# Kernel tuning notes

Measured on AMD Instinct MI355X. Metric: run time of the kernel, lower is better.

The kernel has to match this reference:

```python
import jax, jax.numpy as jnp
import numpy as np

N = 50000        # nodes
E = 800000       # edges (avg degree 16)
D_IN = 128
D_OUT = 128
P_DROP = 0.1
BN_EPS = 1e-5


def setup_inputs() -> dict:
    key = jax.random.key(0)
    k1, k2, k3 = jax.random.split(key, 3)
    x = jax.random.normal(k1, (N, D_IN), dtype=jnp.float32)
    edge_index = jax.random.randint(k2, (2, E), 0, N, dtype=jnp.int64)
    W = jax.random.normal(k3, (D_IN, D_OUT), dtype=jnp.float32) / np.sqrt(D_IN).astype(np.float32)
    b = jnp.zeros((D_OUT,), jnp.float32)
    bn_gamma = jnp.ones((D_OUT,), jnp.float32)
    bn_beta = jnp.zeros((D_OUT,), jnp.float32)
    return {"x": x, "edge_index": edge_index, "W": W, "b": b,
            "bn_gamma": bn_gamma, "bn_beta": bn_beta}


def reference(x, edge_index, W, b, bn_gamma, bn_beta):
    n = x.shape[0]
    # --- GCNConv: h = x W, symmetric-normalized aggregation with self-loops ---
    h = x @ W                                            # [N, D_OUT]
    loops = jnp.arange(n, dtype=edge_index.dtype)
    src = jnp.concatenate([edge_index[0], loops])        # [E+N]
    dst = jnp.concatenate([edge_index[1], loops])        # [E+N]
    deg = jax.ops.segment_sum(jnp.ones_like(dst, h.dtype), dst, num_segments=n)
    dinv = jax.lax.rsqrt(jnp.maximum(deg, 1.0))          # deg >= 1 (self-loops)
    norm = dinv[src] * dinv[dst]                         # [E+N]
    msg = h[src] * norm[:, None]                         # gather + weight
    z = jax.ops.segment_sum(msg, dst, num_segments=n) + b
    # --- activation ---
    z = jax.nn.relu(z)
    # --- BatchNorm over nodes (training-mode batch statistics) ---
    mean = z.mean(axis=0)
    var = z.var(axis=0)
    z = bn_gamma * (z - mean) * jax.lax.rsqrt(var + BN_EPS) + bn_beta
    # --- dropout (training mode, fixed key for determinism) ---
    keep = jax.random.bernoulli(jax.random.key(42), 1.0 - P_DROP, z.shape)
    z = jnp.where(keep, z / (1.0 - P_DROP), 0.0)
    return z.astype(x.dtype)
```

## Files before the change

kernel.cpp:

```cpp
#include <hip/hip_runtime.h>
#include <stdint.h>


#define NN 50000
#define NE 800000
#define DD 128
#define SCAN_B 256
#define NSB ((NN + SCAN_B - 1) / SCAN_B)
#define NSTAT 400

using f32x4  = __attribute__((ext_vector_type(4))) float;
using short8 = __attribute__((ext_vector_type(8))) short;

__device__ __forceinline__ uint32_t rotl32(uint32_t x, uint32_t d) {
  return (x << d) | (x >> (32u - d));
}

__device__ __forceinline__ uint32_t threefry_bits(uint32_t idx) {
  const uint32_t ks0 = 0u;
  const uint32_t ks1 = 42u;
  const uint32_t ks2 = 0x1BD11BDAu ^ ks0 ^ ks1;
  uint32_t x0 = ks0;
  uint32_t x1 = idx + ks1;
#define TF_R(r) { x0 += x1; x1 = rotl32(x1, (r)); x1 ^= x0; }
  TF_R(13u) TF_R(15u) TF_R(26u) TF_R(6u)
  x0 += ks1; x1 += ks2 + 1u;
  TF_R(17u) TF_R(29u) TF_R(16u) TF_R(24u)
  x0 += ks2; x1 += ks0 + 2u;
  TF_R(13u) TF_R(15u) TF_R(26u) TF_R(6u)
  x0 += ks0; x1 += ks1 + 3u;
  TF_R(17u) TF_R(29u) TF_R(16u) TF_R(24u)
  x0 += ks1; x1 += ks2 + 4u;
  TF_R(13u) TF_R(15u) TF_R(26u) TF_R(6u)
  x0 += ks2; x1 += ks0 + 5u;
#undef TF_R
  return x0 ^ x1;
}

__device__ __forceinline__ uint32_t f2bf(float f) {
  uint32_t u = __float_as_uint(f);
  return (u + 0x7fffu + ((u >> 16) & 1u)) >> 16;
}
__device__ __forceinline__ float bf2f(uint32_t h) { return __uint_as_float(h << 16); }
__device__ __forceinline__ float bf_lo(uint32_t p) { return __uint_as_float(p << 16); }
__device__ __forceinline__ float bf_hi(uint32_t p) { return __uint_as_float(p & 0xffff0000u); }

__global__ __launch_bounds__(256) void k_wpack(const float* __restrict__ Wm,
                                               short8* __restrict__ wfh,
                                               short8* __restrict__ wfl) {
  int tid = blockIdx.x * 256 + threadIdx.x;
  if (tid >= 32 * 64) return;
  int lane = tid & 63;
  int cfks = tid >> 6;
  int ks = cfks >> 3, cf = cfks & 7;
  int krow = ks * 32 + ((lane >> 4) << 3);
  int col = cf * 16 + (lane & 15);
  short8 h, l;
#pragma unroll
  for (int j = 0; j < 8; ++j) {
    float w = Wm[(size_t)(krow + j) * DD + col];
    uint32_t hb = f2bf(w);
    uint32_t lb = f2bf(w - bf2f(hb));
    h[j] = (short)hb;
    l[j] = (short)lb;
  }
  wfh[tid] = h;
  wfl[tid] = l;
}

#define GBM 128
__global__ __launch_bounds__(256) void k_gemm(const float* __restrict__ x,
                                              const short8* __restrict__ wfh,
                                              const short8* __restrict__ wfl,
                                              const float* __restrict__ dinv,
                                              uint16_t* __restrict__ hbf) {
  __shared__ uint4 ldsbuf[4096];
  char* lds = (char*)ldsbuf;
  const int t = threadIdx.x;
  const int row0 = blockIdx.x * GBM;
  const int c4 = t & 31, rbase = t >> 5;

#pragma unroll
  for (int i = 0; i < 16; ++i) {
    int r = rbase + i * 8;
    int grow = row0 + r;
    float4 v = make_float4(0.f, 0.f, 0.f, 0.f);
    if (grow < NN)
      v = *reinterpret_cast<const float4*>(&x[(size_t)grow * DD + c4 * 4]);
    uint32_t h0 = f2bf(v.x), h1 = f2bf(v.y), h2 = f2bf(v.z), h3 = f2bf(v.w);
    uint32_t l0 = f2bf(v.x - bf2f(h0)), l1 = f2bf(v.y - bf2f(h1));
    uint32_t l2 = f2bf(v.z - bf2f(h2)), l3 = f2bf(v.w - bf2f(h3));
    int byte = (r * 256 + c4 * 8) ^ ((r & 7) << 4);
    *reinterpret_cast<uint2*>(lds + byte) = make_uint2(h0 | (h1 << 16), h2 | (h3 << 16));
    *reinterpret_cast<uint2*>(lds + 32768 + byte) = make_uint2(l0 | (l1 << 16), l2 | (l3 << 16));
  }
  __syncthreads();

  const int wv = t >> 6, l = t & 63;
  f32x4 acc[2][8] = {};
#pragma unroll
  for (int ks = 0; ks < 4; ++ks) {
    short8 ah[2], al[2];
#pragma unroll
    for (int rf = 0; rf < 2; ++rf) {
      int r = wv * 32 + rf * 16 + (l & 15);
      int byte = (r * 256 + ks * 64 + ((l >> 4) << 4)) ^ ((r & 7) << 4);
      ah[rf] = *reinterpret_cast<const short8*>(lds + byte);
      al[rf] = *reinterpret_cast<const short8*>(lds + 32768 + byte);
    }
#pragma unroll
    for (int cf = 0; cf < 8; ++cf) {
      short8 bh = wfh[(ks * 8 + cf) * 64 + l];
      short8 bl = wfl[(ks * 8 + cf) * 64 + l];
#pragma unroll
      for (int rf = 0; rf < 2; ++rf) {
        acc[rf][cf] = __builtin_amdgcn_mfma_f32_16x16x32_bf16(ah[rf], bl, acc[rf][cf], 0, 0, 0);
        acc[rf][cf] = __builtin_amdgcn_mfma_f32_16x16x32_bf16(al[rf], bh, acc[rf][cf], 0, 0, 0);
        acc[rf][cf] = __builtin_amdgcn_mfma_f32_16x16x32_bf16(ah[rf], bh, acc[rf][cf], 0, 0, 0);
      }
    }
  }
  __syncthreads();

#pragma unroll
  for (int rf = 0; rf < 2; ++rf)
#pragma unroll
    for (int i = 0; i < 4; ++i) {
      int row = wv * 32 + rf * 16 + ((l >> 4) << 2) + i;
      int grow = row0 + row;
      float dv = (grow < NN) ? dinv[grow] : 0.f;
#pragma unroll
      for (int cf = 0; cf < 8; ++cf) {
        int col = cf * 16 + (l & 15);
        int byte = (row * 256 + col * 2) ^ ((row & 7) << 4);
        *reinterpret_cast<uint16_t*>(lds + byte) = (uint16_t)f2bf(acc[rf][cf][i] * dv);
      }
    }
  __syncthreads();
#pragma unroll
  for (int i = 0; i < 16; ++i) {
    int r = rbase + i * 8;
    int grow = row0 + r;
    if (grow < NN) {
      int byte = (r * 256 + c4 * 8) ^ ((r & 7) << 4);
      uint2 v = *reinterpret_cast<const uint2*>(lds + byte);
      *reinterpret_cast<uint2*>(&hbf[(size_t)grow * DD + c4 * 4]) = v;
    }
  }
}

__global__ void k_count(const int* __restrict__ ei, int* __restrict__ cnt,
                        uint16_t* __restrict__ pos) {
  int e = blockIdx.x * blockDim.x + threadIdx.x;
  if (e < NE) pos[e] = (uint16_t)atomicAdd(&cnt[ei[NE + e]], 1);
}

__global__ __launch_bounds__(SCAN_B) void k_scan1(const int* __restrict__ cnt,
                                                  int* __restrict__ tmp,
                                                  int* __restrict__ blk_sums,
                                                  float* __restrict__ dinv) {
  __shared__ int sm[SCAN_B];
  int t = threadIdx.x;
  int i = blockIdx.x * SCAN_B + t;
  int v = (i < NN) ? cnt[i] : 0;
  if (i < NN) dinv[i] = rsqrtf((float)v + 1.0f);
  sm[t] = v;
  __syncthreads();
  for (int off = 1; off < SCAN_B; off <<= 1) {
    int u = (t >= off) ? sm[t - off] : 0;
    __syncthreads();
    sm[t] += u;
    __syncthreads();
  }
  if (i < NN) tmp[i] = sm[t];
  if (t == SCAN_B - 1) blk_sums[blockIdx.x] = sm[t];
}

__global__ __launch_bounds__(SCAN_B) void k_scan3(const int* __restrict__ tmp,
                                                  const int* __restrict__ blk_sums,
                                                  int* __restrict__ row_ptr) {
  __shared__ int sm[SCAN_B];
  int t = threadIdx.x;
  int v = (t < NSB) ? blk_sums[t] : 0;
  sm[t] = v;
  __syncthreads();
  for (int off = 1; off < SCAN_B; off <<= 1) {
    int u = (t >= off) ? sm[t - off] : 0;
    __syncthreads();
    sm[t] += u;
    __syncthreads();
  }
  int excl = sm[blockIdx.x] - blk_sums[blockIdx.x];
  int i = blockIdx.x * SCAN_B + t;
  if (i < NN) {
    row_ptr[i + 1] = tmp[i] + excl;
    if (i == 0) row_ptr[0] = 0;
  }
}

__global__ void k_fill(const int* __restrict__ ei, const int* __restrict__ row_ptr,
                       const uint16_t* __restrict__ pos, uint16_t* __restrict__ colv) {
  int e = blockIdx.x * blockDim.x + threadIdx.x;
  if (e < NE) {
    int d = ei[NE + e];
    colv[row_ptr[d] + (int)pos[e]] = (uint16_t)ei[e];
  }
}

__global__ __launch_bounds__(256) void k_agg(const uint16_t* __restrict__ hbf,
                                             const int* __restrict__ row_ptr,
                                             const uint16_t* __restrict__ colv,
                                             const float* __restrict__ dinv,
                                             const float* __restrict__ bias,
                                             float* __restrict__ z) {
  int wave = threadIdx.x >> 6;
  int lane = threadIdx.x & 63;
  int node = blockIdx.x * 4 + wave;
  if (node >= NN) return;
  const uint32_t* hp = reinterpret_cast<const uint32_t*>(hbf);

  uint32_t ms = hp[(size_t)node * 64 + lane];
  float ax = bf_lo(ms), ay = bf_hi(ms);

  int e = row_ptr[node], end = row_ptr[node + 1];
  while (e + 16 <= end) {
    int s[16]; uint32_t m[16];
#pragma unroll
    for (int q = 0; q < 16; ++q) s[q] = colv[e + q];
#pragma unroll
    for (int q = 0; q < 16; ++q) m[q] = hp[(size_t)s[q] * 64 + lane];
#pragma unroll
    for (int q = 0; q < 16; ++q) {
      ax += bf_lo(m[q]);
      ay += bf_hi(m[q]);
    }
    e += 16;
  }
  while (e + 8 <= end) {
    int s[8]; uint32_t m[8];
#pragma unroll
    for (int q = 0; q < 8; ++q) s[q] = colv[e + q];
#pragma unroll
    for (int q = 0; q < 8; ++q) m[q] = hp[(size_t)s[q] * 64 + lane];
#pragma unroll
    for (int q = 0; q < 8; ++q) {
      ax += bf_lo(m[q]);
      ay += bf_hi(m[q]);
    }
    e += 8;
  }
  while (e < end) {
    uint32_t m0 = hp[(size_t)colv[e] * 64 + lane];
    ax += bf_lo(m0);
    ay += bf_hi(m0);
    ++e;
  }
  float di = dinv[node];
  float2 bb = reinterpret_cast<const float2*>(bias)[lane];
  float zx = fmaxf(fmaf(ax, di, bb.x), 0.f);
  float zy = fmaxf(fmaf(ay, di, bb.y), 0.f);
  reinterpret_cast<float2*>(z)[(size_t)node * 64 + lane] = make_float2(zx, zy);
}

__global__ __launch_bounds__(256) void k_stats(const float* __restrict__ z,
                                               float* __restrict__ part) {
  int t = threadIdx.x;
  int c4 = t & 31;
  int rgrp = t >> 5;
  float sx = 0.f, sy = 0.f, sz = 0.f, sw = 0.f;
  float qx = 0.f, qy = 0.f, qz = 0.f, qw = 0.f;
  for (int r = blockIdx.x * 8 + rgrp; r < NN; r += NSTAT * 8) {
    float4 v = *reinterpret_cast<const float4*>(&z[(size_t)r * DD + c4 * 4]);
    sx += v.x; sy += v.y; sz += v.z; sw += v.w;
    qx = fmaf(v.x, v.x, qx); qy = fmaf(v.y, v.y, qy);
    qz = fmaf(v.z, v.z, qz); qw = fmaf(v.w, v.w, qw);
  }
  __shared__ float sm[2048], sm2[2048];
  sm[t * 4 + 0] = sx; sm[t * 4 + 1] = sy; sm[t * 4 + 2] = sz; sm[t * 4 + 3] = sw;
  sm2[t * 4 + 0] = qx; sm2[t * 4 + 1] = qy; sm2[t * 4 + 2] = qz; sm2[t * 4 + 3] = qw;
  __syncthreads();
  int c = t & 127;
  float acc = 0.f;
  if (t < 128) {
#pragma unroll
    for (int g = 0; g < 8; ++g) acc += sm[g * 128 + c];
  } else {
#pragma unroll
    for (int g = 0; g < 8; ++g) acc += sm2[g * 128 + c];
  }
  part[blockIdx.x * 256 + t] = acc;
}

__global__ __launch_bounds__(256) void k_stats2(const float* __restrict__ part,
                                                float* __restrict__ bn_sum,
                                                float* __restrict__ bn_sumsq) {
  int t = threadIdx.x;
  float acc = 0.f;
  for (int b = 0; b < NSTAT; ++b) acc += part[b * 256 + t];
  if (t < 128) bn_sum[t] = acc;
  else bn_sumsq[t - 128] = acc;
}

__global__ __launch_bounds__(256) void k_final(float* __restrict__ z,
                                               const float* __restrict__ bn_sum,
                                               const float* __restrict__ bn_sumsq,
                                               const float* __restrict__ gamma,
                                               const float* __restrict__ beta) {
  int j4 = blockIdx.x * blockDim.x + threadIdx.x;
  if (j4 >= NN * DD / 4) return;
  int c4 = j4 & 31;
  const float invN = 1.0f / (float)NN;
  float4 s = *reinterpret_cast<const float4*>(&bn_sum[c4 * 4]);
  float4 q = *reinterpret_cast<const float4*>(&bn_sumsq[c4 * 4]);
  float4 g = *reinterpret_cast<const float4*>(&gamma[c4 * 4]);
  float4 bt = *reinterpret_cast<const float4*>(&beta[c4 * 4]);
  float4 v = *reinterpret_cast<const float4*>(&z[(size_t)j4 * 4]);
  float out[4];
  float mm[4] = {s.x * invN, s.y * invN, s.z * invN, s.w * invN};
  float qq[4] = {q.x * invN, q.y * invN, q.z * invN, q.w * invN};
  float gg[4] = {g.x, g.y, g.z, g.w};
  float bb[4] = {bt.x, bt.y, bt.z, bt.w};
  float vv[4] = {v.x, v.y, v.z, v.w};
#pragma unroll
  for (int i = 0; i < 4; ++i) {
    float var = qq[i] - mm[i] * mm[i];
    float rs = rsqrtf(var + 1e-5f);
    float val = (vv[i] - mm[i]) * rs * gg[i] + bb[i];
    uint32_t bits = threefry_bits((uint32_t)(j4 * 4 + i));
    float u = __uint_as_float((bits >> 9) | 0x3f800000u) - 1.0f;
    out[i] = (u < 0.9f) ? val * (1.0f / 0.9f) : 0.0f;
  }
  *reinterpret_cast<float4*>(&z[(size_t)j4 * 4]) = make_float4(out[0], out[1], out[2], out[3]);
}

extern "C" void kernel_launch(void* const* d_in, const int* in_sizes, int n_in,
                              void* d_out, int out_size, void* d_ws, size_t ws_size,
                              hipStream_t stream) {
  const float* x     = (const float*)d_in[0];
  const int*   ei    = (const int*)d_in[1];
  const float* Wm    = (const float*)d_in[2];
  const float* bvec  = (const float*)d_in[3];
  const float* gamma = (const float*)d_in[4];
  const float* beta  = (const float*)d_in[5];
  float* zout = (float*)d_out;

  uint16_t* hbf  = (uint16_t*)d_ws;
  short8* wfh    = (short8*)(hbf + (size_t)NN * DD);
  short8* wfl    = wfh + 2048;
  uint16_t* colv = (uint16_t*)(wfl + 2048);
  uint16_t* pos  = colv + NE;
  int* cnt       = (int*)(pos + NE);
  float* bn_sum  = (float*)(cnt + NN);
  float* bn_sumsq= bn_sum + DD;
  int* tmp_scan  = (int*)(bn_sumsq + DD);
  int* row_ptr   = tmp_scan + NN;
  float* dinv    = (float*)(row_ptr + NN + 1);
  int* blk_sums  = (int*)(dinv + NN);
  float* part    = (float*)(blk_sums + NSB);

  hipMemsetAsync(cnt, 0, (size_t)NN * sizeof(int), stream);

  k_wpack<<<8, 256, 0, stream>>>(Wm, wfh, wfl);
  k_count<<<(NE + 255) / 256, 256, 0, stream>>>(ei, cnt, pos);
  k_scan1<<<NSB, SCAN_B, 0, stream>>>(cnt, tmp_scan, blk_sums, dinv);
  k_scan3<<<NSB, SCAN_B, 0, stream>>>(tmp_scan, blk_sums, row_ptr);
  k_gemm<<<(NN + GBM - 1) / GBM, 256, 0, stream>>>(x, wfh, wfl, dinv, hbf);
  k_fill<<<(NE + 255) / 256, 256, 0, stream>>>(ei, row_ptr, pos, colv);
  k_agg<<<(NN + 3) / 4, 256, 0, stream>>>(hbf, row_ptr, colv, dinv, bvec, zout);
  k_stats<<<NSTAT, 256, 0, stream>>>(zout, part);
  k_stats2<<<1, 256, 0, stream>>>(part, bn_sum, bn_sumsq);
  k_final<<<(NN * DD / 4 + 255) / 256, 256, 0, stream>>>(zout, bn_sum, bn_sumsq, gamma, beta);
}
```

Before: 160.5 us.

## Fuse launches with last-block tickets and a grid-wide spin barrier

Cuts the number of launches. The memset and weight packing are merged into one setup kernel. The two scan kernels become one, where the last-arriving block finalizes row_ptr. Stats, reduction and normalize/dropout are fused into a persistent BN kernel that uses an atomic ticket and a spin-wait flag. The count and fill kernels also handle two edges per thread with packed positions. The grid-wide spin relies on all 256 blocks being co-resident, and the single last block serially writes all of row_ptr, which may be slow.

```diff
diff --git a/kernel.cpp b/kernel.cpp
--- a/kernel.cpp
+++ b/kernel.cpp
@@ -7,7 +7,7 @@
 #define DD 128
 #define SCAN_B 256
 #define NSB ((NN + SCAN_B - 1) / SCAN_B)
-#define NSTAT 400
+#define NSTAT 256
 
 using f32x4  = __attribute__((ext_vector_type(4))) float;
 using short8 = __attribute__((ext_vector_type(8))) short;
@@ -45,27 +45,36 @@
 __device__ __forceinline__ float bf_lo(uint32_t p) { return __uint_as_float(p << 16); }
 __device__ __forceinline__ float bf_hi(uint32_t p) { return __uint_as_float(p & 0xffff0000u); }
 
-__global__ __launch_bounds__(256) void k_wpack(const float* __restrict__ Wm,
+__global__ __launch_bounds__(256) void k_setup(const float* __restrict__ Wm,
                                                short8* __restrict__ wfh,
-                                               short8* __restrict__ wfl) {
-  int tid = blockIdx.x * 256 + threadIdx.x;
-  if (tid >= 32 * 64) return;
-  int lane = tid & 63;
-  int cfks = tid >> 6;
-  int ks = cfks >> 3, cf = cfks & 7;
-  int krow = ks * 32 + ((lane >> 4) << 3);
-  int col = cf * 16 + (lane & 15);
-  short8 h, l;
-#pragma unroll
-  for (int j = 0; j < 8; ++j) {
-    float w = Wm[(size_t)(krow + j) * DD + col];
-    uint32_t hb = f2bf(w);
-    uint32_t lb = f2bf(w - bf2f(hb));
-    h[j] = (short)hb;
-    l[j] = (short)lb;
-  }
-  wfh[tid] = h;
-  wfl[tid] = l;
+                                               short8* __restrict__ wfl,
+                                               int* __restrict__ cnt,
+                                               int* __restrict__ sync) {
+  int b = blockIdx.x;
+  int t = threadIdx.x;
+  if (b < 8) {
+    int tid = b * 256 + t;
+    int lane = tid & 63;
+    int cfks = tid >> 6;
+    int ks = cfks >> 3, cf = cfks & 7;
+    int krow = ks * 32 + ((lane >> 4) << 3);
+    int col = cf * 16 + (lane & 15);
+    short8 h, l;
+#pragma unroll
+    for (int j = 0; j < 8; ++j) {
+      float w = Wm[(size_t)(krow + j) * DD + col];
+      uint32_t hb = f2bf(w);
+      uint32_t lb = f2bf(w - bf2f(hb));
+      h[j] = (short)hb;
+      l[j] = (short)lb;
+    }
+    wfh[tid] = h;
+    wfl[tid] = l;
+  } else {
+    int i = (b - 8) * 256 + t;
+    if (i < NN) cnt[i] = 0;
+    if (b == 8 && t < 4) sync[t] = 0;
+  }
 }
 
 #define GBM 128
@@ -150,16 +159,26 @@
 }
 
 __global__ void k_count(const int* __restrict__ ei, int* __restrict__ cnt,
-                        uint16_t* __restrict__ pos) {
-  int e = blockIdx.x * blockDim.x + threadIdx.x;
-  if (e < NE) pos[e] = (uint16_t)atomicAdd(&cnt[ei[NE + e]], 1);
-}
-
-__global__ __launch_bounds__(SCAN_B) void k_scan1(const int* __restrict__ cnt,
-                                                  int* __restrict__ tmp,
-                                                  int* __restrict__ blk_sums,
-                                                  float* __restrict__ dinv) {
+                        uint32_t* __restrict__ pos2) {
+  int e2 = blockIdx.x * blockDim.x + threadIdx.x;
+  int e = e2 * 2;
+  if (e < NE) {
+    int2 d = *reinterpret_cast<const int2*>(&ei[NE + e]);
+    uint32_t p0 = (uint32_t)atomicAdd(&cnt[d.x], 1) & 0xffffu;
+    uint32_t p1 = (uint32_t)atomicAdd(&cnt[d.y], 1) & 0xffffu;
+    pos2[e2] = p0 | (p1 << 16);
+  }
+}
+
+__global__ __launch_bounds__(SCAN_B) void k_scan(const int* __restrict__ cnt,
+                                                 int* __restrict__ tmp,
+                                                 int* __restrict__ blk_sums,
+                                                 float* __restrict__ dinv,
+                                                 int* __restrict__ row_ptr,
+                                                 int* __restrict__ sync) {
   __shared__ int sm[SCAN_B];
+  __shared__ int excl[SCAN_B];
+  __shared__ int ticket_s;
   int t = threadIdx.x;
   int i = blockIdx.x * SCAN_B + t;
   int v = (i < NN) ? cnt[i] : 0;
@@ -174,15 +193,16 @@
   }
   if (i < NN) tmp[i] = sm[t];
   if (t == SCAN_B - 1) blk_sums[blockIdx.x] = sm[t];
-}
-
-__global__ __launch_bounds__(SCAN_B) void k_scan3(const int* __restrict__ tmp,
-                                                  const int* __restrict__ blk_sums,
-                                                  int* __restrict__ row_ptr) {
-  __shared__ int sm[SCAN_B];
-  int t = threadIdx.x;
-  int v = (t < NSB) ? blk_sums[t] : 0;
-  sm[t] = v;
+  __threadfence();
+  __syncthreads();
+  if (t == 0) ticket_s = atomicAdd(&sync[0], 1);
+  __syncthreads();
+  if (ticket_s != NSB - 1) return;
+
+  __threadfence();
+  int bv = (t < NSB) ? blk_sums[t] : 0;
+  __syncthreads();
+  sm[t] = bv;
   __syncthreads();
   for (int off = 1; off < SCAN_B; off <<= 1) {
     int u = (t >= off) ? sm[t - off] : 0;
@@ -190,20 +210,25 @@
     sm[t] += u;
     __syncthreads();
   }
-  int excl = sm[blockIdx.x] - blk_sums[blockIdx.x];
-  int i = blockIdx.x * SCAN_B + t;
-  if (i < NN) {
-    row_ptr[i + 1] = tmp[i] + excl;
-    if (i == 0) row_ptr[0] = 0;
-  }
+  excl[t] = sm[t] - bv;
+  __syncthreads();
+  for (int base = 0; base < NN; base += SCAN_B) {
+    int idx = base + t;
+    if (idx < NN) row_ptr[idx + 1] = tmp[idx] + excl[idx >> 8];
+  }
+  if (t == 0) row_ptr[0] = 0;
 }
 
 __global__ void k_fill(const int* __restrict__ ei, const int* __restrict__ row_ptr,
-                       const uint16_t* __restrict__ pos, uint16_t* __restrict__ colv) {
-  int e = blockIdx.x * blockDim.x + threadIdx.x;
+                       const uint32_t* __restrict__ pos2, uint16_t* __restrict__ colv) {
+  int e2 = blockIdx.x * blockDim.x + threadIdx.x;
+  int e = e2 * 2;
   if (e < NE) {
-    int d = ei[NE + e];
-    colv[row_ptr[d] + (int)pos[e]] = (uint16_t)ei[e];
+    int2 s = *reinterpret_cast<const int2*>(&ei[e]);
+    int2 d = *reinterpret_cast<const int2*>(&ei[NE + e]);
+    uint32_t pp = pos2[e2];
+    colv[row_ptr[d.x] + (int)(pp & 0xffffu)] = (uint16_t)s.x;
+    colv[row_ptr[d.y] + (int)(pp >> 16)]     = (uint16_t)s.y;
   }
 }
 
@@ -262,75 +287,99 @@
   reinterpret_cast<float2*>(z)[(size_t)node * 64 + lane] = make_float2(zx, zy);
 }
 
-__global__ __launch_bounds__(256) void k_stats(const float* __restrict__ z,
-                                               float* __restrict__ part) {
+__global__ __launch_bounds__(256) void k_bn(float* __restrict__ z,
+                                            float* __restrict__ part,
+                                            float* __restrict__ bn_sum,
+                                            float* __restrict__ bn_sumsq,
+                                            const float* __restrict__ gamma,
+                                            const float* __restrict__ beta,
+                                            int* __restrict__ sync) {
   int t = threadIdx.x;
-  int c4 = t & 31;
-  int rgrp = t >> 5;
-  float sx = 0.f, sy = 0.f, sz = 0.f, sw = 0.f;
-  float qx = 0.f, qy = 0.f, qz = 0.f, qw = 0.f;
-  for (int r = blockIdx.x * 8 + rgrp; r < NN; r += NSTAT * 8) {
-    float4 v = *reinterpret_cast<const float4*>(&z[(size_t)r * DD + c4 * 4]);
-    sx += v.x; sy += v.y; sz += v.z; sw += v.w;
-    qx = fmaf(v.x, v.x, qx); qy = fmaf(v.y, v.y, qy);
-    qz = fmaf(v.z, v.z, qz); qw = fmaf(v.w, v.w, qw);
-  }
-  __shared__ float sm[2048], sm2[2048];
-  sm[t * 4 + 0] = sx; sm[t * 4 + 1] = sy; sm[t * 4 + 2] = sz; sm[t * 4 + 3] = sw;
-  sm2[t * 4 + 0] = qx; sm2[t * 4 + 1] = qy; sm2[t * 4 + 2] = qz; sm2[t * 4 + 3] = qw;
-  __syncthreads();
-  int c = t & 127;
-  float acc = 0.f;
-  if (t < 128) {
-#pragma unroll
-    for (int g = 0; g < 8; ++g) acc += sm[g * 128 + c];
+  {
+    int c4 = t & 31;
+    int rgrp = t >> 5;
+    float sx = 0.f, sy = 0.f, sz = 0.f, sw = 0.f;
+    float qx = 0.f, qy = 0.f, qz = 0.f, qw = 0.f;
+    for (int r = blockIdx.x * 8 + rgrp; r < NN; r += NSTAT * 8) {
+      float4 v = *reinterpret_cast<const float4*>(&z[(size_t)r * DD + c4 * 4]);
+      sx += v.x; sy += v.y; sz += v.z; sw += v.w;
+      qx = fmaf(v.x, v.x, qx); qy = fmaf(v.y, v.y, qy);
+      qz = fmaf(v.z, v.z, qz); qw = fmaf(v.w, v.w, qw);
+    }
+    __shared__ float sm[2048], sm2[2048];
+    sm[t * 4 + 0] = sx; sm[t * 4 + 1] = sy; sm[t * 4 + 2] = sz; sm[t * 4 + 3] = sw;
+    sm2[t * 4 + 0] = qx; sm2[t * 4 + 1] = qy; sm2[t * 4 + 2] = qz; sm2[t * 4 + 3] = qw;
+    __syncthreads();
+    int c = t & 127;
+    float acc = 0.f;
+    if (t < 128) {
+#pragma unroll
+      for (int g = 0; g < 8; ++g) acc += sm[g * 128 + c];
+    } else {
+#pragma unroll
+      for (int g = 0; g < 8; ++g) acc += sm2[g * 128 + c];
+    }
+    part[blockIdx.x * 256 + t] = acc;
+  }
+  __threadfence();
+  __syncthreads();
+  __shared__ int ticket_s;
+  if (t == 0) ticket_s = atomicAdd(&sync[1], 1);
+  __syncthreads();
+  if (ticket_s == NSTAT - 1) {
+    __threadfence();
+    float a = 0.f;
+    for (int b = 0; b < NSTAT; ++b) a += part[b * 256 + t];
+    if (t < 128) bn_sum[t] = a;
+    else bn_sumsq[t - 128] = a;
+    __threadfence();
+    __syncthreads();
+    if (t == 0) atomicExch(&sync[2], 1);
   } else {
-#pragma unroll
-    for (int g = 0; g < 8; ++g) acc += sm2[g * 128 + c];
-  }
-  part[blockIdx.x * 256 + t] = acc;
-}
-
-__global__ __launch_bounds__(256) void k_stats2(const float* __restrict__ part,
-                                                float* __restrict__ bn_sum,
-                                                float* __restrict__ bn_sumsq) {
-  int t = threadIdx.x;
-  float acc = 0.f;
-  for (int b = 0; b < NSTAT; ++b) acc += part[b * 256 + t];
-  if (t < 128) bn_sum[t] = acc;
-  else bn_sumsq[t - 128] = acc;
-}
-
-__global__ __launch_bounds__(256) void k_final(float* __restrict__ z,
-                                               const float* __restrict__ bn_sum,
-                                               const float* __restrict__ bn_sumsq,
-                                               const float* __restrict__ gamma,
-                                               const float* __restrict__ beta) {
-  int j4 = blockIdx.x * blockDim.x + threadIdx.x;
-  if (j4 >= NN * DD / 4) return;
-  int c4 = j4 & 31;
+    if (t == 0) {
+      while (__hip_atomic_load(&sync[2], __ATOMIC_ACQUIRE, __HIP_MEMORY_SCOPE_AGENT) == 0)
+        __builtin_amdgcn_s_sleep(10);
+    }
+    __syncthreads();
+  }
+  __threadfence();
+
   const float invN = 1.0f / (float)NN;
-  float4 s = *reinterpret_cast<const float4*>(&bn_sum[c4 * 4]);
-  float4 q = *reinterpret_cast<const float4*>(&bn_sumsq[c4 * 4]);
-  float4 g = *reinterpret_cast<const float4*>(&gamma[c4 * 4]);
-  float4 bt = *reinterpret_cast<const float4*>(&beta[c4 * 4]);
-  float4 v = *reinterpret_cast<const float4*>(&z[(size_t)j4 * 4]);
-  float out[4];
-  float mm[4] = {s.x * invN, s.y * invN, s.z * invN, s.w * invN};
-  float qq[4] = {q.x * invN, q.y * invN, q.z * invN, q.w * invN};
-  float gg[4] = {g.x, g.y, g.z, g.w};
-  float bb[4] = {bt.x, bt.y, bt.z, bt.w};
-  float vv[4] = {v.x, v.y, v.z, v.w};
-#pragma unroll
-  for (int i = 0; i < 4; ++i) {
-    float var = qq[i] - mm[i] * mm[i];
-    float rs = rsqrtf(var + 1e-5f);
-    float val = (vv[i] - mm[i]) * rs * gg[i] + bb[i];
-    uint32_t bits = threefry_bits((uint32_t)(j4 * 4 + i));
-    float u = __uint_as_float((bits >> 9) | 0x3f800000u) - 1.0f;
-    out[i] = (u < 0.9f) ? val * (1.0f / 0.9f) : 0.0f;
-  }
-  *reinterpret_cast<float4*>(&z[(size_t)j4 * 4]) = make_float4(out[0], out[1], out[2], out[3]);
+  int c4p = -1;
+  float mm[4], rr[4], gg[4], bb[4];
+  for (int j4 = blockIdx.x * 256 + t; j4 < NN * DD / 4; j4 += NSTAT * 256) {
+    int c4 = j4 & 31;
+    if (c4 != c4p) {
+      c4p = c4;
+      float4 s = *reinterpret_cast<const float4*>(&bn_sum[c4 * 4]);
+      float4 q = *reinterpret_cast<const float4*>(&bn_sumsq[c4 * 4]);
+      float4 g = *reinterpret_cast<const float4*>(&gamma[c4 * 4]);
+      float4 bt = *reinterpret_cast<const float4*>(&beta[c4 * 4]);
+      float sv[4] = {s.x, s.y, s.z, s.w};
+      float qv[4] = {q.x, q.y, q.z, q.w};
+      float gv[4] = {g.x, g.y, g.z, g.w};
+      float bv[4] = {bt.x, bt.y, bt.z, bt.w};
+#pragma unroll
+      for (int i = 0; i < 4; ++i) {
+        mm[i] = sv[i] * invN;
+        float var = qv[i] * invN - mm[i] * mm[i];
+        rr[i] = rsqrtf(var + 1e-5f) * gv[i];
+        bb[i] = bv[i];
+        gg[i] = 0.f; (void)gg;
+      }
+    }
+    float4 v = *reinterpret_cast<const float4*>(&z[(size_t)j4 * 4]);
+    float vv[4] = {v.x, v.y, v.z, v.w};
+    float out[4];
+#pragma unroll
+    for (int i = 0; i < 4; ++i) {
+      float val = (vv[i] - mm[i]) * rr[i] + bb[i];
+      uint32_t bits = threefry_bits((uint32_t)(j4 * 4 + i));
+      float u = __uint_as_float((bits >> 9) | 0x3f800000u) - 1.0f;
+      out[i] = (u < 0.9f) ? val * (1.0f / 0.9f) : 0.0f;
+    }
+    *reinterpret_cast<float4*>(&z[(size_t)j4 * 4]) = make_float4(out[0], out[1], out[2], out[3]);
+  }
 }
 
 extern "C" void kernel_launch(void* const* d_in, const int* in_sizes, int n_in,
@@ -348,8 +397,8 @@
   short8* wfh    = (short8*)(hbf + (size_t)NN * DD);
   short8* wfl    = wfh + 2048;
   uint16_t* colv = (uint16_t*)(wfl + 2048);
-  uint16_t* pos  = colv + NE;
-  int* cnt       = (int*)(pos + NE);
+  uint32_t* pos2 = (uint32_t*)(colv + NE);
+  int* cnt       = (int*)(pos2 + NE / 2);
   float* bn_sum  = (float*)(cnt + NN);
   float* bn_sumsq= bn_sum + DD;
   int* tmp_scan  = (int*)(bn_sumsq + DD);
@@ -357,17 +406,13 @@
   float* dinv    = (float*)(row_ptr + NN + 1);
   int* blk_sums  = (int*)(dinv + NN);
   float* part    = (float*)(blk_sums + NSB);
-
-  hipMemsetAsync(cnt, 0, (size_t)NN * sizeof(int), stream);
-
-  k_wpack<<<8, 256, 0, stream>>>(Wm, wfh, wfl);
-  k_count<<<(NE + 255) / 256, 256, 0, stream>>>(ei, cnt, pos);
-  k_scan1<<<NSB, SCAN_B, 0, stream>>>(cnt, tmp_scan, blk_sums, dinv);
-  k_scan3<<<NSB, SCAN_B, 0, stream>>>(tmp_scan, blk_sums, row_ptr);
+  int* sync      = (int*)(part + NSTAT * 256);
+
+  k_setup<<<8 + NSB, 256, 0, stream>>>(Wm, wfh, wfl, cnt, sync);
+  k_count<<<(NE / 2 + 255) / 256, 256, 0, stream>>>(ei, cnt, pos2);
+  k_scan<<<NSB, SCAN_B, 0, stream>>>(cnt, tmp_scan, blk_sums, dinv, row_ptr, sync);
   k_gemm<<<(NN + GBM - 1) / GBM, 256, 0, stream>>>(x, wfh, wfl, dinv, hbf);
-  k_fill<<<(NE + 255) / 256, 256, 0, stream>>>(ei, row_ptr, pos, colv);
+  k_fill<<<(NE / 2 + 255) / 256, 256, 0, stream>>>(ei, row_ptr, pos2, colv);
   k_agg<<<(NN + 3) / 4, 256, 0, stream>>>(hbf, row_ptr, colv, dinv, bvec, zout);
-  k_stats<<<NSTAT, 256, 0, stream>>>(zout, part);
-  k_stats2<<<1, 256, 0, stream>>>(part, bn_sum, bn_sumsq);
-  k_final<<<(NN * DD / 4 + 255) / 256, 256, 0, stream>>>(zout, bn_sum, bn_sumsq, gamma, beta);
-}
+  k_bn<<<NSTAT, 256, 0, stream>>>(zout, part, bn_sum, bn_sumsq, gamma, beta, sync);
+}
```

New measurement: 293.2 us. 1.83x slower.
